# Performance work log

Measured on AMD Instinct MI355X. Metric: run time of the kernel, lower is better.

Reference implementation:

```python
import jax, jax.numpy as jnp
import numpy as np

B, C, E, HLR, WLR = 2, 64, 4, 192, 192


def setup_inputs() -> dict:
    key = jax.random.key(0)
    ks = jax.random.split(key, 8)
    s = 0.05  # keep activations/offsets in a sane range
    return {
        "x": jax.random.normal(ks[0], (B, C, HLR, WLR), jnp.float32),
        "fused": jax.random.normal(ks[1], (B, C, HLR, WLR), jnp.float32),
        "weight_compress": jax.random.normal(ks[2], (E, C // 8, C), jnp.float32) * s,
        "weight_expand": jax.random.normal(ks[3], (E, C, C // 8), jnp.float32) * s,
        "body_w1": jax.random.normal(ks[4], (64, 4), jnp.float32) * s,
        "body_b1": jnp.zeros((64,), jnp.float32),
        "body_w2": jax.random.normal(ks[5], (64, 64), jnp.float32) * s,
        "body_b2": jnp.zeros((64,), jnp.float32),
        "routing_w": jax.random.normal(ks[6], (E, 64), jnp.float32) * s,
        "routing_b": jnp.zeros((E,), jnp.float32),
        "offset_w": jax.random.normal(ks[7], (2, 64), jnp.float32) * s,
        "offset_b": jnp.zeros((2,), jnp.float32),
        "scale": 2,
    }


def _conv1x1(x, w, b):
    # x: [n, cin, H, W], w: [cout, cin] (1x1 conv)
    return jnp.einsum('oc,nchw->nohw', w, x) + b[None, :, None, None]


def _grid_sample(img, px, py):
    # Bilinear sample, align_corners=True semantics, zeros padding.
    # img: [b,c,h,w]; px, py: [b,H,W] absolute LR pixel coords.
    b, c, h, w = img.shape
    x0 = jnp.floor(px)
    y0 = jnp.floor(py)
    wx = (px - x0)[:, None]  # [b,1,H,W]
    wy = (py - y0)[:, None]

    def gather(xi, yi):
        valid = (xi >= 0) & (xi <= w - 1) & (yi >= 0) & (yi <= h - 1)
        xc = jnp.clip(xi, 0, w - 1).astype(jnp.int32)
        yc = jnp.clip(yi, 0, h - 1).astype(jnp.int32)
        v = jax.vmap(lambda im, yy, xx: im[:, yy, xx])(img, yc, xc)  # [b,c,H,W]
        return v * valid[:, None].astype(img.dtype)

    v00 = gather(x0, y0)
    v01 = gather(x0 + 1, y0)
    v10 = gather(x0, y0 + 1)
    v11 = gather(x0 + 1, y0 + 1)
    top = v00 * (1 - wx) + v01 * wx
    bot = v10 * (1 - wx) + v11 * wx
    return top * (1 - wy) + bot * wy


def reference(x, fused, weight_compress, weight_expand, body_w1, body_b1,
              body_w2, body_b2, routing_w, routing_b, offset_w, offset_b, scale):
    b, c, h, w = fused.shape
    H, W = round(h * scale), round(w * scale)
    e, c8 = weight_compress.shape[0], weight_compress.shape[1]

    ch = jnp.arange(H, dtype=jnp.float32)
    cw = jnp.arange(W, dtype=jnp.float32)
    coor_h = (ch + 0.5) / scale - jnp.floor((ch + 0.5) / scale + 0.001) - 0.5  # [H]
    coor_w = (cw + 0.5) / scale - jnp.floor((cw + 0.5) / scale + 0.001) - 0.5  # [W]
    inp = jnp.stack([
        jnp.full((H, W), 1.0 / scale, jnp.float32),
        jnp.full((H, W), 1.0 / scale, jnp.float32),
        jnp.broadcast_to(coor_h[:, None], (H, W)),
        jnp.broadcast_to(coor_w[None, :], (H, W)),
    ], 0)[None]  # [1,4,H,W]

    emb = jax.nn.relu(_conv1x1(inp, body_w1, body_b1))
    emb = jax.nn.relu(_conv1x1(emb, body_w2, body_b2))
    offset = _conv1x1(emb, offset_w, offset_b)            # [1,2,H,W]
    routing = jax.nn.sigmoid(_conv1x1(emb, routing_w, routing_b))  # [1,E,H,W]

    rw = routing.reshape(e, H * W).T                      # [HW, E]
    wc = (rw @ weight_compress.reshape(e, -1)).reshape(H, W, c8, c)  # per-pixel compress
    we = (rw @ weight_expand.reshape(e, -1)).reshape(H, W, c, c8)    # per-pixel expand

    # deformable sample: HR grid projected into LR space + learned offset (pixel units)
    px = jnp.broadcast_to((cw[None, :] + 0.5) / scale - 0.5, (H, W))[None] + offset[:, 0]
    py = jnp.broadcast_to((ch[:, None] + 0.5) / scale - 0.5, (H, W))[None] + offset[:, 1]
    px = jnp.broadcast_to(px, (b, H, W))
    py = jnp.broadcast_to(py, (b, H, W))
    fea0 = _grid_sample(fused, px, py)                    # [b,c,H,W]

    fea = fea0.transpose(0, 2, 3, 1)                      # [b,H,W,c]
    mid = jnp.einsum('hwoc,bhwc->bhwo', wc, fea)          # [b,H,W,c//8]
    out = jnp.einsum('hwco,bhwo->bhwc', we, mid)          # [b,H,W,c]
    return out.transpose(0, 3, 1, 2) + fea0
```

## Files before the change

kernel.cpp:

```cpp
#include <hip/hip_runtime.h>
#include <math.h>

typedef __attribute__((ext_vector_type(8))) short short8;
typedef __attribute__((ext_vector_type(4))) float f32x4;

#define HLR_ 192
#define WLR_ 192
#define H_ 384
#define W_ 384
#define LRP (HLR_*WLR_)
#define PTILES (LRP/64)
#define TPX 128
#define NTW (W_/TPX)

#define WS_K_OFF 4718592
#define WS_OFF_OFF (WS_K_OFF + 8192)

__device__ __forceinline__ unsigned short f32_bf16(float x){
    union { float f; unsigned int u; } v; v.f = x;
    unsigned int r = v.u + 0x7fffu + ((v.u >> 16) & 1u);
    return (unsigned short)(r >> 16);
}
__device__ __forceinline__ float bf16_f32(unsigned short h){
    union { float f; unsigned int u; } v; v.u = ((unsigned int)h) << 16;
    return v.f;
}

__global__ __launch_bounds__(256) void precompute_kernel(
    const float* __restrict__ w1, const float* __restrict__ b1,
    const float* __restrict__ w2, const float* __restrict__ b2,
    const float* __restrict__ rw, const float* __restrict__ rb,
    const float* __restrict__ ow, const float* __restrict__ ob,
    const float* __restrict__ WC, const float* __restrict__ WE,
    unsigned short* __restrict__ Kmat, float* __restrict__ g_off)
{
    __shared__ float sW2[64*65];
    __shared__ float sRW[6*64];
    __shared__ float sE1[4][64];
    __shared__ float sR[4][4];
    __shared__ float sWc[4][8][64];
    __shared__ float sWe[4][64][8];

    int tid = threadIdx.x;
    for (int idx = tid; idx < 4096; idx += 256)
        sW2[(idx>>6)*65 + (idx&63)] = w2[idx];
    if (tid < 256) sRW[tid] = rw[tid];
    if (tid < 128) sRW[256 + tid] = ow[tid];

    int wave = tid >> 6, lane = tid & 63;
    int ph = wave >> 1, pw = wave & 1;

    float ch = (ph + 0.5f)*0.5f;
    float coor_h = ch - floorf(ch + 0.001f) - 0.5f;
    float cw = (pw + 0.5f)*0.5f;
    float coor_w = cw - floorf(cw + 0.001f) - 0.5f;

    float e1 = w1[lane*4+0]*0.5f + w1[lane*4+1]*0.5f
             + w1[lane*4+2]*coor_h + w1[lane*4+3]*coor_w + b1[lane];
    sE1[wave][lane] = fmaxf(e1, 0.0f);
    __syncthreads();

    float e2 = b2[lane];
    #pragma unroll 16
    for (int i = 0; i < 64; ++i) e2 += sW2[lane*65 + i] * sE1[wave][i];
    e2 = fmaxf(e2, 0.0f);

    #pragma unroll
    for (int k = 0; k < 6; ++k) {
        float t = sRW[k*64 + lane] * e2;
        #pragma unroll
        for (int m = 1; m <= 32; m <<= 1) t += __shfl_xor(t, m, 64);
        if (lane == 0) {
            if (k < 4) sR[wave][k] = 1.0f/(1.0f + expf(-(t + rb[k])));
            else       g_off[wave*2 + (k-4)] = t + ob[k-4];
        }
    }
    __syncthreads();

    for (int idx = tid; idx < 2048; idx += 256) {
        int cls = idx >> 9, rem = idx & 511;
        float r0=sR[cls][0], r1=sR[cls][1], r2=sR[cls][2], r3=sR[cls][3];
        sWc[cls][rem>>6][rem&63] =
            r0*WC[0*512+rem] + r1*WC[1*512+rem] + r2*WC[2*512+rem] + r3*WC[3*512+rem];
    }
    for (int idx = tid; idx < 2048; idx += 256) {
        int cls = idx >> 9, rem = idx & 511;
        float r0=sR[cls][0], r1=sR[cls][1], r2=sR[cls][2], r3=sR[cls][3];
        sWe[cls][rem>>3][rem&7] =
            r0*WE[0*512+rem] + r1*WE[1*512+rem] + r2*WE[2*512+rem] + r3*WE[3*512+rem];
    }
    __syncthreads();

    for (int idx = tid; idx < 16384; idx += 256) {
        int cls = idx >> 12, rem = idx & 4095;
        int c = rem >> 6, cp = rem & 63;
        float a = 0.0f;
        #pragma unroll
        for (int o = 0; o < 8; ++o) a += sWe[cls][c][o] * sWc[cls][o][cp];
        Kmat[idx] = f32_bf16(a);
    }
}

__global__ __launch_bounds__(256) void transpose_kernel(
    const float* __restrict__ fused, float* __restrict__ fused_t)
{
    __shared__ float tile[64][65];
    int bid = blockIdx.x;
    int b = bid / PTILES, pt = bid % PTILES;
    int p0 = pt * 64;
    int tid = threadIdx.x;
    int tlo = tid & 63, thi = tid >> 6;
    #pragma unroll
    for (int i = 0; i < 16; ++i) {
        int c = thi + i*4;
        tile[c][tlo] = fused[(size_t)(b*64 + c)*LRP + p0 + tlo];
    }
    __syncthreads();
    #pragma unroll
    for (int i = 0; i < 16; ++i) {
        int p = thi + i*4;
        fused_t[(size_t)(b*LRP + p0 + p)*64 + tlo] = tile[tlo][p];
    }
}

__global__ __launch_bounds__(256, 2) void main_kernel(
    const float* __restrict__ fused_t, const unsigned short* __restrict__ Kmat,
    const float* __restrict__ g_off, float* __restrict__ out)
{
    __shared__ unsigned short sFea[256*72];

    int bid = blockIdx.x;
    int h = bid / NTW, wt = bid % NTW;
    int w0 = wt * TPX;
    int tid = threadIdx.x, wave = tid >> 6, lane = tid & 63;
    int b = wave >> 1, par = wave & 1;
    int ph = h & 1, cls = ph*2 + par;

    float off0 = g_off[cls*2 + 0];
    float off1 = g_off[cls*2 + 1];

    float py  = (h + 0.5f)*0.5f - 0.5f + off1;
    float y0f = floorf(py);
    float wy  = py - y0f;
    int   y0  = (int)y0f;
    float fy0 = (y0 >= 0  && y0 <= HLR_-1) ? 1.0f : 0.0f;
    float fy1 = (y0 >= -1 && y0 <= HLR_-2) ? 1.0f : 0.0f;
    int   yc0 = min(max(y0, 0), HLR_-1);
    int   yc1 = min(max(y0+1, 0), HLR_-1);
    float omwy = 1.0f - wy;

    float pxb  = (w0 + par + 0.5f)*0.5f - 0.5f + off0;
    float x0bf = floorf(pxb);
    float wx   = pxb - x0bf;
    int   x0b  = (int)x0bf;
    float omwx = 1.0f - wx;

    const float* baseB = fused_t + (size_t)b * LRP * 64;
    const float* r0 = baseB + (size_t)yc0 * WLR_ * 64;
    const float* r1 = baseB + (size_t)yc1 * WLR_ * 64;
    unsigned short* sRow = sFea + wave*64*72;

    #pragma unroll 8
    for (int i = 0; i < 64; ++i) {
        int x0 = x0b + i;
        float fx0 = (x0 >= 0  && x0 <= WLR_-1) ? 1.0f : 0.0f;
        float fx1 = (x0 >= -1 && x0 <= WLR_-2) ? 1.0f : 0.0f;
        int xc0 = min(max(x0, 0), WLR_-1);
        int xc1 = min(max(x0+1, 0), WLR_-1);
        float w00 = omwx*omwy*fx0*fy0;
        float w01 = wx  *omwy*fx1*fy0;
        float w10 = omwx*wy  *fx0*fy1;
        float w11 = wx  *wy  *fx1*fy1;
        float v = r0[xc0*64 + lane]*w00 + r0[xc1*64 + lane]*w01
                + r1[xc0*64 + lane]*w10 + r1[xc1*64 + lane]*w11;
        sRow[i*72 + lane] = f32_bf16(v);
    }
    __syncthreads();

    int lm = lane & 15, lg = lane >> 4;

    short8 Bf[2][4];
    #pragma unroll
    for (int nt = 0; nt < 4; ++nt)
        #pragma unroll
        for (int kt = 0; kt < 2; ++kt)
            Bf[kt][nt] = *(const short8*)(sFea + (wave*64 + nt*16 + lm)*72 + kt*32 + lg*8);

    const unsigned short* Kc = Kmat + cls*4096;
    short8 Af[4][2];
    #pragma unroll
    for (int mt = 0; mt < 4; ++mt)
        #pragma unroll
        for (int kt = 0; kt < 2; ++kt)
            Af[mt][kt] = *(const short8*)(Kc + (mt*16 + lm)*64 + kt*32 + lg*8);

    f32x4 acc[4][4];
    #pragma unroll
    for (int mt = 0; mt < 4; ++mt) {
        #pragma unroll
        for (int nt = 0; nt < 4; ++nt) {
            f32x4 a = {0.0f, 0.0f, 0.0f, 0.0f};
            a = __builtin_amdgcn_mfma_f32_16x16x32_bf16(Af[mt][0], Bf[0][nt], a, 0, 0, 0);
            a = __builtin_amdgcn_mfma_f32_16x16x32_bf16(Af[mt][1], Bf[1][nt], a, 0, 0, 0);
            acc[mt][nt] = a;
        }
    }

    #pragma unroll
    for (int mt = 0; mt < 4; ++mt) {
        #pragma unroll
        for (int nt = 0; nt < 4; ++nt) {
            int slot = wave*64 + nt*16 + lm;
            ushort4 idv = *(const ushort4*)(sFea + slot*72 + mt*16 + lg*4);
            int wc = w0 + 2*(nt*16 + lm) + par;
            int c0 = mt*16 + lg*4;
            float* op = out + (((size_t)(b*64 + c0)*H_ + h)*W_ + wc);
            op[0*(size_t)(H_*W_)] = acc[mt][nt][0] + bf16_f32(idv.x);
            op[1*(size_t)(H_*W_)] = acc[mt][nt][1] + bf16_f32(idv.y);
            op[2*(size_t)(H_*W_)] = acc[mt][nt][2] + bf16_f32(idv.z);
            op[3*(size_t)(H_*W_)] = acc[mt][nt][3] + bf16_f32(idv.w);
        }
    }
}

extern "C" void kernel_launch(void* const* d_in, const int* in_sizes, int n_in,
                              void* d_out, int out_size, void* d_ws, size_t ws_size,
                              hipStream_t stream)
{
    const float* fused = (const float*)d_in[1];
    const float* WC    = (const float*)d_in[2];
    const float* WE    = (const float*)d_in[3];
    const float* w1    = (const float*)d_in[4];
    const float* b1    = (const float*)d_in[5];
    const float* w2    = (const float*)d_in[6];
    const float* b2    = (const float*)d_in[7];
    const float* rw    = (const float*)d_in[8];
    const float* rb    = (const float*)d_in[9];
    const float* ow    = (const float*)d_in[10];
    const float* ob    = (const float*)d_in[11];
    (void)in_sizes; (void)n_in; (void)out_size; (void)ws_size;

    float* ws = (float*)d_ws;
    float* fused_t = ws;
    unsigned short* Kmat = (unsigned short*)(ws + WS_K_OFF);
    float* g_off = ws + WS_OFF_OFF;
    float* o = (float*)d_out;

    hipLaunchKernelGGL(precompute_kernel, dim3(1), dim3(256), 0, stream,
                       w1, b1, w2, b2, rw, rb, ow, ob, WC, WE, Kmat, g_off);
    hipLaunchKernelGGL(transpose_kernel, dim3(2*PTILES), dim3(256), 0, stream,
                       fused, fused_t);
    hipLaunchKernelGGL(main_kernel, dim3(H_*NTW), dim3(256), 0, stream,
                       fused_t, Kmat, g_off, o);
}
```

Before: 164.6 us.

## Vectorize bilinear gather, remap blocks by XCD, raise occupancy bound

The gather loop now has each lane load float4 chunks of four channels, with four sample items per wave iteration instead of one scalar channel per lane. Stores to LDS become 8-byte writes. Blocks are remapped so that each of the 8 XCDs handles a contiguous band of 48 output rows, which is meant to improve L2 reuse of LR rows. Launch bounds rise from 2 to 4 blocks per SM, which could cap registers and cause spills in the MFMA section.

```diff
diff --git a/kernel.cpp b/kernel.cpp
--- a/kernel.cpp
+++ b/kernel.cpp
@@ -123,14 +123,18 @@
     }
 }
 
-__global__ __launch_bounds__(256, 2) void main_kernel(
+__global__ __launch_bounds__(256, 4) void main_kernel(
     const float* __restrict__ fused_t, const unsigned short* __restrict__ Kmat,
     const float* __restrict__ g_off, float* __restrict__ out)
 {
     __shared__ unsigned short sFea[256*72];
 
-    int bid = blockIdx.x;
-    int h = bid / NTW, wt = bid % NTW;
+    int g = blockIdx.x;
+    int xcd = g & 7;
+    int t = g >> 3;
+    int q = t / 3;
+    int wt = t - q*3;
+    int h = xcd*48 + q;
     int w0 = wt * TPX;
     int tid = threadIdx.x, wave = tid >> 6, lane = tid & 63;
     int b = wave >> 1, par = wave & 1;
@@ -155,25 +159,35 @@
     int   x0b  = (int)x0bf;
     float omwx = 1.0f - wx;
 
+    float W00 = omwx*omwy*fy0, W01 = wx*omwy*fy0;
+    float W10 = omwx*wy  *fy1, W11 = wx*wy  *fy1;
+
+    int itg = lane >> 4;
+    int cg  = lane & 15;
+
     const float* baseB = fused_t + (size_t)b * LRP * 64;
-    const float* r0 = baseB + (size_t)yc0 * WLR_ * 64;
-    const float* r1 = baseB + (size_t)yc1 * WLR_ * 64;
-    unsigned short* sRow = sFea + wave*64*72;
-
-    #pragma unroll 8
-    for (int i = 0; i < 64; ++i) {
-        int x0 = x0b + i;
+    const float* r0 = baseB + (size_t)yc0 * WLR_ * 64 + cg*4;
+    const float* r1 = baseB + (size_t)yc1 * WLR_ * 64 + cg*4;
+    unsigned short* sW = sFea + wave*64*72 + cg*4;
+
+    #pragma unroll
+    for (int j = 0; j < 16; ++j) {
+        int item = j*4 + itg;
+        int x0 = x0b + item;
         float fx0 = (x0 >= 0  && x0 <= WLR_-1) ? 1.0f : 0.0f;
         float fx1 = (x0 >= -1 && x0 <= WLR_-2) ? 1.0f : 0.0f;
         int xc0 = min(max(x0, 0), WLR_-1);
         int xc1 = min(max(x0+1, 0), WLR_-1);
-        float w00 = omwx*omwy*fx0*fy0;
-        float w01 = wx  *omwy*fx1*fy0;
-        float w10 = omwx*wy  *fx0*fy1;
-        float w11 = wx  *wy  *fx1*fy1;
-        float v = r0[xc0*64 + lane]*w00 + r0[xc1*64 + lane]*w01
-                + r1[xc0*64 + lane]*w10 + r1[xc1*64 + lane]*w11;
-        sRow[i*72 + lane] = f32_bf16(v);
+        float a00 = W00*fx0, a01 = W01*fx1, a10 = W10*fx0, a11 = W11*fx1;
+        f32x4 v00 = *(const f32x4*)(r0 + (size_t)xc0*64);
+        f32x4 v01 = *(const f32x4*)(r0 + (size_t)xc1*64);
+        f32x4 v10 = *(const f32x4*)(r1 + (size_t)xc0*64);
+        f32x4 v11 = *(const f32x4*)(r1 + (size_t)xc1*64);
+        f32x4 v = v00*a00 + v01*a01 + v10*a10 + v11*a11;
+        ushort4 u;
+        u.x = f32_bf16(v[0]); u.y = f32_bf16(v[1]);
+        u.z = f32_bf16(v[2]); u.w = f32_bf16(v[3]);
+        *(ushort4*)(sW + item*72) = u;
     }
     __syncthreads();
 
```

After: 155.8 us. 1.06x faster.
